# Kernel tuning notes

Hardware: AMD Instinct MI355X
Metric: run time of the kernel (lower is better)

The kernel has to match this reference:

```python
import jax, jax.numpy as jnp
import numpy as np

D_MODEL, D_K, D_V, HEADS = 512, 8, 8, 6
EPS = 1e-5


def setup_inputs() -> dict:
    key = jax.random.key(0)
    ks = jax.random.split(key, 16)
    B, S = 16, 1024
    inp = {
        'q_input': jax.random.normal(ks[0], (B, S, D_MODEL), jnp.float32),
        'k_input': jax.random.normal(ks[1], (B, S, D_MODEL), jnp.float32),
        'v_input': jax.random.normal(ks[2], (B, S, D_MODEL), jnp.float32),
        'mask': jax.random.randint(ks[3], (B, S, S), 0, 2).astype(bool),
        'Wq': jax.random.normal(ks[4], (D_MODEL, D_K * HEADS), jnp.float32) * 0.04,
        'bq': jax.random.normal(ks[5], (D_K * HEADS,), jnp.float32) * 0.02,
        'Wk': jax.random.normal(ks[6], (D_MODEL, D_K * HEADS), jnp.float32) * 0.04,
        'bk': jax.random.normal(ks[7], (D_K * HEADS,), jnp.float32) * 0.02,
        'Wv': jax.random.normal(ks[8], (D_MODEL, D_V * HEADS), jnp.float32) * 0.04,
        'bv': jax.random.normal(ks[9], (D_V * HEADS,), jnp.float32) * 0.02,
        'Wo': jax.random.normal(ks[10], (HEADS * D_K, D_MODEL), jnp.float32) * 0.1,
        'bo': jax.random.normal(ks[11], (D_MODEL,), jnp.float32) * 0.02,
        'ln_w': 1.0 + jax.random.normal(ks[12], (D_MODEL,), jnp.float32) * 0.02,
        'ln_b': jax.random.normal(ks[13], (D_MODEL,), jnp.float32) * 0.02,
    }
    return inp


def reference(q_input, k_input, v_input, mask, Wq, bq, Wk, bk, Wv, bv, Wo, bo, ln_w, ln_b):
    B, S, _ = q_input.shape
    # projections -> [B, H, S, d]
    q_s = (q_input @ Wq + bq).reshape(B, S, HEADS, D_K).transpose(0, 2, 1, 3)
    k_s = (k_input @ Wk + bk).reshape(B, S, HEADS, D_K).transpose(0, 2, 1, 3)
    v_s = (v_input @ Wv + bv).reshape(B, S, HEADS, D_V).transpose(0, 2, 1, 3)
    # scaled dot-product with masked_fill(mask, 1e-9) as in the original (fills VALUE, not -inf)
    scores = jnp.einsum('bhqd,bhkd->bhqk', q_s, k_s) / np.sqrt(D_K).astype(np.float32)
    scores = jnp.where(mask[:, None, :, :], jnp.float32(1e-9), scores)
    attn = jax.nn.softmax(scores, axis=-1)
    out = jnp.einsum('bhqk,bhkd->bhqd', attn, v_s)  # [B,H,S,d_v]
    out = out.transpose(0, 2, 1, 3).reshape(B, S, HEADS * D_K)
    out = out @ Wo + bo
    x = q_input + out  # residual
    mu = jnp.mean(x, axis=-1, keepdims=True)
    var = jnp.var(x, axis=-1, keepdims=True)
    return (x - mu) * jax.lax.rsqrt(var + EPS) * ln_w + ln_b
```

## Files before the change

kernel.cpp:

```cpp
#include <hip/hip_runtime.h>

constexpr int B = 16;
constexpr int S = 1024;
constexpr int DM = 512;
constexpr int H = 6;
constexpr int DK = 8;
constexpr int NJ = H * DK;
constexpr int BS = B * S;
constexpr int WB_ELEMS = 16 * NJ * 32;

typedef __attribute__((ext_vector_type(8))) short bf16x8;
typedef __attribute__((ext_vector_type(8))) _Float16 half8;
typedef __attribute__((ext_vector_type(4))) _Float16 half4;
typedef __attribute__((ext_vector_type(4))) float floatx4;

#define LOG2E 1.4426950408889634f
#define QSCALE (0.35355339059327373f * LOG2E)

__device__ inline ushort f2bf(float f) {
  unsigned int u = __builtin_bit_cast(unsigned int, f);
  return (ushort)((u + 0x7FFFu + ((u >> 16) & 1u)) >> 16);
}

__global__ __launch_bounds__(256) void maskbits_kernel(
    const int* __restrict__ mask, unsigned long long* __restrict__ bits) {
  int wave = threadIdx.x >> 6, lane = threadIdx.x & 63;
  int row = blockIdx.x * 4 + wave;
  const int* mrow = mask + (size_t)row * S;
  unsigned long long* brow = bits + (size_t)row * 16;
  int koff = ((lane >> 5) << 5) + 2 * (lane & 15) + ((lane >> 4) & 1);
#pragma unroll
  for (int c = 0; c < 16; c++) {
    int v = mrow[c * 64 + koff];
    unsigned long long bal = __ballot(v != 0);
    if (lane == 0) brow[c] = bal;
  }
}

__global__ __launch_bounds__(256) void wprep_kernel(
    const float* __restrict__ Wq, const float* __restrict__ Wk,
    const float* __restrict__ Wv, ushort* __restrict__ Wb,
    uint2* __restrict__ VBf) {
  int m = blockIdx.x;
  if (m < 3) {
    const float* W = (m == 0) ? Wq : (m == 1) ? Wk : Wv;
    ushort* dst = Wb + (size_t)m * WB_ELEMS;
    for (int e = threadIdx.x; e < WB_ELEMS; e += 256) {
      int kc = e / 1536;
      int rem = e - kc * 1536;
      int n = rem >> 5, kj = rem & 31;
      dst[e] = f2bf(W[(size_t)(kc * 32 + kj) * NJ + n]);
    }
  } else {
    int bh = m - 3;
    for (int i = threadIdx.x; i < 2048; i += 256) {
      int tile = i >> 5;
      int li = i & 31;
      int g = li >> 3, dd = 8 + (li & 7);
      uint hv = (dd == 8) ? 0x3C003C00u : 0u;
      uint2 val; val.x = hv; val.y = hv;
      VBf[((size_t)bh * 64 + tile) * 64 + g * 16 + dd] = val;
    }
  }
}

__global__ __launch_bounds__(256) void proj_kernel(
    const float* __restrict__ q_in, const float* __restrict__ k_in,
    const float* __restrict__ v_in, const ushort* __restrict__ Wb,
    const float* __restrict__ bq, const float* __restrict__ bk,
    const float* __restrict__ bv,
    ushort* __restrict__ Qo, ushort* __restrict__ Ko, ushort* __restrict__ Vo) {
  int m = blockIdx.y;
  const float* x    = (m == 0) ? q_in : (m == 1) ? k_in : v_in;
  const float* bias = (m == 0) ? bq   : (m == 1) ? bk   : bv;
  ushort* out       = (m == 0) ? Qo   : (m == 1) ? Ko   : Vo;
  float oscale      = (m == 0) ? QSCALE : 1.0f;
  const ushort* Wg  = Wb + (size_t)m * WB_ELEMS;

  __shared__ ushort Wl[WB_ELEMS];

  int t = threadIdx.x;
  {
    const uint4* src = (const uint4*)Wg;
    uint4* dst = (uint4*)Wl;
#pragma unroll
    for (int i = 0; i < 12; i++) dst[t + i * 256] = src[t + i * 256];
  }

  int r0 = blockIdx.x * 64;
  int wave = t >> 6, lane = t & 63;
  int n16 = lane & 15, quad = lane >> 4;
  const float* xrow = x + (size_t)(r0 + wave * 16 + n16) * DM + quad * 8;

  floatx4 acc0 = {0.f, 0.f, 0.f, 0.f};
  floatx4 acc1 = {0.f, 0.f, 0.f, 0.f};
  floatx4 acc2 = {0.f, 0.f, 0.f, 0.f};

  __syncthreads();

#pragma unroll 4
  for (int kc = 0; kc < 16; kc++) {
    float4 xa = *(const float4*)(xrow + kc * 32);
    float4 xb = *(const float4*)(xrow + kc * 32 + 4);
    bf16x8 a;
    a[0] = (short)f2bf(xa.x); a[1] = (short)f2bf(xa.y);
    a[2] = (short)f2bf(xa.z); a[3] = (short)f2bf(xa.w);
    a[4] = (short)f2bf(xb.x); a[5] = (short)f2bf(xb.y);
    a[6] = (short)f2bf(xb.z); a[7] = (short)f2bf(xb.w);
    const ushort* wbase = &Wl[(kc * 48 + n16) * 32 + quad * 8];
    bf16x8 b0 = *(const bf16x8*)(wbase);
    bf16x8 b1 = *(const bf16x8*)(wbase + 16 * 32);
    bf16x8 b2 = *(const bf16x8*)(wbase + 32 * 32);
    acc0 = __builtin_amdgcn_mfma_f32_16x16x32_bf16(a, b0, acc0, 0, 0, 0);
    acc1 = __builtin_amdgcn_mfma_f32_16x16x32_bf16(a, b1, acc1, 0, 0, 0);
    acc2 = __builtin_amdgcn_mfma_f32_16x16x32_bf16(a, b2, acc2, 0, 0, 0);
  }

  int baseR = r0 + wave * 16 + quad * 4;
#pragma unroll
  for (int j = 0; j < 3; j++) {
    floatx4 a = (j == 0) ? acc0 : (j == 1) ? acc1 : acc2;
    int n = j * 16 + n16;
    float bn = bias[n];
    int h = n >> 3, d = n & 7;
#pragma unroll
    for (int r = 0; r < 4; r++) {
      int R = baseR + r;
      int b = R >> 10, s = R & 1023;
      float fv = (a[r] + bn) * oscale;
      if (m == 2) {
        size_t idx =
            ((((size_t)(b * H + h) * 64 + (s >> 4)) * 64) +
             ((s >> 2) & 3) * 16 + d) * 4 + (s & 3);
        out[idx] = __builtin_bit_cast(ushort, (_Float16)fv);
      } else {
        out[(((size_t)(b * H + h)) * S + s) * 8 + d] = f2bf(fv);
      }
    }
  }
}

__global__ __launch_bounds__(256, 6) void attn_kernel(
    const ushort* __restrict__ Qg, const ushort* __restrict__ Kg,
    const ushort* __restrict__ VBg ,
    const uint* __restrict__ bits32, float* __restrict__ A) {
  int bh = blockIdx.x >> 4;
  int qt = blockIdx.x & 15;
  int b = bh / H, h = bh % H;
  int q0 = qt * 64;

  int t = threadIdx.x;
  int wave = t >> 6, lane = t & 63;
  int quad = lane >> 4, n16 = lane & 15;

  const ushort* Kbase = Kg + (size_t)bh * S * 8;
  const uint2* VB = (const uint2*)VBg + (size_t)bh * (64 * 64);

  bf16x8 aq = {0, 0, 0, 0, 0, 0, 0, 0};
  if (quad == 0)
    aq = *(const bf16x8*)&Qg[((size_t)bh * S + q0 + wave * 16 + n16) * 8];

  const uint* mrow = bits32 + (size_t)(b * S + q0 + wave * 16 + n16) * 32;

  floatx4 acc0 = {0.f, 0.f, 0.f, 0.f};
  floatx4 acc1 = {0.f, 0.f, 0.f, 0.f};
  const floatx4 zero = {0.f, 0.f, 0.f, 0.f};
  int sh0 = 2 * quad;

#pragma unroll 1
  for (int cc = 0; cc < 8; cc++) {
    uint4 mq = *(const uint4*)(mrow + cc * 4);
#pragma unroll
    for (int ci = 0; ci < 4; ci++) {
      int c = cc * 4 + ci;
      uint mw = (ci == 0) ? mq.x : (ci == 1) ? mq.y : (ci == 2) ? mq.z : mq.w;

      bf16x8 ak0 = *(const bf16x8*)&Kbase[(size_t)(c * 32 + n16) * 8];
      bf16x8 ak1 = *(const bf16x8*)&Kbase[(size_t)(c * 32 + 16 + n16) * 8];
      uint2 vb0 = VB[(2 * c) * 64 + lane];
      uint2 vb1 = VB[(2 * c + 1) * 64 + lane];

      floatx4 s0 = __builtin_amdgcn_mfma_f32_16x16x32_bf16(ak0, aq, zero, 0, 0, 0);
      floatx4 s1 = __builtin_amdgcn_mfma_f32_16x16x32_bf16(ak1, aq, zero, 0, 0, 0);

      float p0 = exp2f(fminf(s0[0], 15.f)), p1 = exp2f(fminf(s0[1], 15.f));
      float p2 = exp2f(fminf(s0[2], 15.f)), p3 = exp2f(fminf(s0[3], 15.f));
      float p4 = exp2f(fminf(s1[0], 15.f)), p5 = exp2f(fminf(s1[1], 15.f));
      float p6 = exp2f(fminf(s1[2], 15.f)), p7 = exp2f(fminf(s1[3], 15.f));
      uint w0 = __builtin_bit_cast(uint, __builtin_amdgcn_cvt_pkrtz(p0, p1));
      uint w1 = __builtin_bit_cast(uint, __builtin_amdgcn_cvt_pkrtz(p2, p3));
      uint w2 = __builtin_bit_cast(uint, __builtin_amdgcn_cvt_pkrtz(p4, p5));
      uint w3 = __builtin_bit_cast(uint, __builtin_amdgcn_cvt_pkrtz(p6, p7));

      uint m0 = ((mw >> sh0) & 0x10001u) * 0xFFFFu;
      uint m1 = ((mw >> (sh0 + 1)) & 0x10001u) * 0xFFFFu;
      uint m2 = ((mw >> (sh0 + 8)) & 0x10001u) * 0xFFFFu;
      uint m3 = ((mw >> (sh0 + 9)) & 0x10001u) * 0xFFFFu;
      w0 = (m0 & 0x3C003C00u) | (~m0 & w0);
      w1 = (m1 & 0x3C003C00u) | (~m1 & w1);
      w2 = (m2 & 0x3C003C00u) | (~m2 & w2);
      w3 = (m3 & 0x3C003C00u) | (~m3 & w3);

      uint2 pu0; pu0.x = w0; pu0.y = w1;
      uint2 pu1; pu1.x = w2; pu1.y = w3;
      half4 pa0 = __builtin_bit_cast(half4, pu0);
      half4 pa1 = __builtin_bit_cast(half4, pu1);

      acc0 = __builtin_amdgcn_mfma_f32_16x16x16f16(
          pa0, __builtin_bit_cast(half4, vb0), acc0, 0, 0, 0);
      acc1 = __builtin_amdgcn_mfma_f32_16x16x16f16(
          pa1, __builtin_bit_cast(half4, vb1), acc1, 0, 0, 0);
    }
  }

#pragma unroll
  for (int r = 0; r < 4; r++) {
    float sum = acc0[r] + acc1[r];
    float dnm = __shfl(sum, (lane & 48) | 8, 64);
    if (n16 < 8) {
      int qg = q0 + wave * 16 + quad * 4 + r;
      A[((size_t)(b * S + qg)) * NJ + h * 8 + n16] = sum / dnm;
    }
  }
}

__global__ __launch_bounds__(256) void out_ln_kernel(
    const float* __restrict__ A, const float* __restrict__ Wo,
    const float* __restrict__ bo, const float* __restrict__ qin,
    const float* __restrict__ lnw, const float* __restrict__ lnb,
    float* __restrict__ out) {
  int r0 = blockIdx.x * 8;
  int t = threadIdx.x;
  __shared__ float As[8 * NJ];
#pragma unroll
  for (int i = t; i < 8 * NJ; i += 256) As[i] = A[(size_t)r0 * NJ + i];
  __syncthreads();

  int c0 = t, c1 = t + 256;
  float acc0[8], acc1[8];
#pragma unroll
  for (int r = 0; r < 8; r++) { acc0[r] = 0.f; acc1[r] = 0.f; }

#pragma unroll 4
  for (int j = 0; j < NJ; j++) {
    float w0 = Wo[(size_t)j * DM + c0];
    float w1 = Wo[(size_t)j * DM + c1];
#pragma unroll
    for (int r = 0; r < 8; r++) {
      float a = As[r * NJ + j];
      acc0[r] += a * w0;
      acc1[r] += a * w1;
    }
  }

  float b0 = bo[c0], b1 = bo[c1];
  float y0[8], y1[8], ssum[8], sq[8];
#pragma unroll
  for (int r = 0; r < 8; r++) {
    y0[r] = acc0[r] + b0 + qin[(size_t)(r0 + r) * DM + c0];
    y1[r] = acc1[r] + b1 + qin[(size_t)(r0 + r) * DM + c1];
    ssum[r] = y0[r] + y1[r];
    sq[r] = y0[r] * y0[r] + y1[r] * y1[r];
  }

  int wave = t >> 6, lane = t & 63;
  __shared__ float reds[4][8], redq[4][8];
#pragma unroll
  for (int r = 0; r < 8; r++) {
    float s = ssum[r], qq = sq[r];
#pragma unroll
    for (int off = 32; off > 0; off >>= 1) {
      s += __shfl_xor(s, off, 64);
      qq += __shfl_xor(qq, off, 64);
    }
    if (lane == 0) { reds[wave][r] = s; redq[wave][r] = qq; }
  }
  __syncthreads();

  float lw0 = lnw[c0], lw1 = lnw[c1], lb0 = lnb[c0], lb1 = lnb[c1];
#pragma unroll
  for (int r = 0; r < 8; r++) {
    float s = (reds[0][r] + reds[1][r]) + (reds[2][r] + reds[3][r]);
    float qq = (redq[0][r] + redq[1][r]) + (redq[2][r] + redq[3][r]);
    float mu = s * (1.f / 512.f);
    float var = qq * (1.f / 512.f) - mu * mu;
    float rstd = rsqrtf(var + 1e-5f);
    out[(size_t)(r0 + r) * DM + c0] = (y0[r] - mu) * rstd * lw0 + lb0;
    out[(size_t)(r0 + r) * DM + c1] = (y1[r] - mu) * rstd * lw1 + lb1;
  }
}

extern "C" void kernel_launch(void* const* d_in, const int* in_sizes, int n_in,
                              void* d_out, int out_size, void* d_ws,
                              size_t ws_size, hipStream_t stream) {
  const float* q_in = (const float*)d_in[0];
  const float* k_in = (const float*)d_in[1];
  const float* v_in = (const float*)d_in[2];
  const int* mask = (const int*)d_in[3];
  const float* Wq = (const float*)d_in[4];
  const float* bq = (const float*)d_in[5];
  const float* Wk = (const float*)d_in[6];
  const float* bk = (const float*)d_in[7];
  const float* Wv = (const float*)d_in[8];
  const float* bv = (const float*)d_in[9];
  const float* Wo = (const float*)d_in[10];
  const float* bo = (const float*)d_in[11];
  const float* lnw = (const float*)d_in[12];
  const float* lnb = (const float*)d_in[13];
  float* out = (float*)d_out;

  constexpr size_t QKV = (size_t)B * H * S * DK;
  ushort* base = (ushort*)d_ws;
  ushort* Qw = base;
  ushort* Kw = base + QKV;
  ushort* VBw = base + 2 * QKV;
  float* Aw = (float*)(base + 4 * QKV);
  unsigned long long* bits = (unsigned long long*)(Aw + (size_t)BS * NJ);
  ushort* Wb = (ushort*)(bits + (size_t)BS * 16);

  maskbits_kernel<<<BS / 4, 256, 0, stream>>>(mask, bits);
  wprep_kernel<<<3 + B * H, 256, 0, stream>>>(Wq, Wk, Wv, Wb, (uint2*)VBw);
  proj_kernel<<<dim3(BS / 64, 3), 256, 0, stream>>>(
      q_in, k_in, v_in, Wb, bq, bk, bv, Qw, Kw, VBw);
  attn_kernel<<<(B * H * S) / 64, 256, 0, stream>>>(
      Qw, Kw, VBw, (const uint*)bits, Aw);
  out_ln_kernel<<<BS / 8, 256, 0, stream>>>(Aw, Wo, bo, q_in, lnw, lnb, out);
}
```

Before: 305.9 us.

## Stage K/V tiles in LDS for attention and prefetch activations in projection

The attention kernel now copies the whole per-head K (16 KB) and V (32 KB) block into shared memory once per workgroup and reads from LDS in the inner loop, replacing repeated global/L2 reads. The inner loop is also fully unrolled. Occupancy hint drops from 6 to 3 blocks per CU to fit the 48 KB of LDS. The projection kernel software-prefetches activation rows four steps ahead, issuing the first loads before the weight copy to overlap latency. The trade-offs are lower occupancy and a serial load phase before compute in attention.

New measurement: 307.5 us. Within noise of the previous version (+0.5%).

```diff
diff --git a/kernel.cpp b/kernel.cpp
--- a/kernel.cpp
+++ b/kernel.cpp
@@ -80,28 +80,39 @@
   __shared__ ushort Wl[WB_ELEMS];
 
   int t = threadIdx.x;
-  {
-    const uint4* src = (const uint4*)Wg;
-    uint4* dst = (uint4*)Wl;
-#pragma unroll
-    for (int i = 0; i < 12; i++) dst[t + i * 256] = src[t + i * 256];
-  }
-
   int r0 = blockIdx.x * 64;
   int wave = t >> 6, lane = t & 63;
   int n16 = lane & 15, quad = lane >> 4;
   const float* xrow = x + (size_t)(r0 + wave * 16 + n16) * DM + quad * 8;
 
+  float4 pa[4], pb[4];
+#pragma unroll
+  for (int i = 0; i < 4; i++) {
+    pa[i] = *(const float4*)(xrow + i * 32);
+    pb[i] = *(const float4*)(xrow + i * 32 + 4);
+  }
+
+  {
+    const uint4* src = (const uint4*)Wg;
+    uint4* dst = (uint4*)Wl;
+#pragma unroll
+    for (int i = 0; i < 12; i++) dst[t + i * 256] = src[t + i * 256];
+  }
+
   floatx4 acc0 = {0.f, 0.f, 0.f, 0.f};
   floatx4 acc1 = {0.f, 0.f, 0.f, 0.f};
   floatx4 acc2 = {0.f, 0.f, 0.f, 0.f};
 
   __syncthreads();
 
-#pragma unroll 4
+#pragma unroll
   for (int kc = 0; kc < 16; kc++) {
-    float4 xa = *(const float4*)(xrow + kc * 32);
-    float4 xb = *(const float4*)(xrow + kc * 32 + 4);
+    float4 xa = pa[kc & 3];
+    float4 xb = pb[kc & 3];
+    if (kc + 4 < 16) {
+      pa[kc & 3] = *(const float4*)(xrow + (kc + 4) * 32);
+      pb[kc & 3] = *(const float4*)(xrow + (kc + 4) * 32 + 4);
+    }
     bf16x8 a;
     a[0] = (short)f2bf(xa.x); a[1] = (short)f2bf(xa.y);
     a[2] = (short)f2bf(xa.z); a[3] = (short)f2bf(xa.w);
@@ -140,7 +151,7 @@
   }
 }
 
-__global__ __launch_bounds__(256, 6) void attn_kernel(
+__global__ __launch_bounds__(256, 3) void attn_kernel(
     const ushort* __restrict__ Qg, const ushort* __restrict__ Kg,
     const ushort* __restrict__ VBg ,
     const uint* __restrict__ bits32, float* __restrict__ A) {
@@ -149,25 +160,39 @@
   int b = bh / H, h = bh % H;
   int q0 = qt * 64;
 
+  __shared__ uint4 Kl[1024];
+  __shared__ uint2 Vl[64 * 64];
+
   int t = threadIdx.x;
   int wave = t >> 6, lane = t & 63;
   int quad = lane >> 4, n16 = lane & 15;
 
-  const ushort* Kbase = Kg + (size_t)bh * S * 8;
-  const uint2* VB = (const uint2*)VBg + (size_t)bh * (64 * 64);
+  {
+    const uint4* Ksrc = (const uint4*)(Kg + (size_t)bh * S * 8);
+#pragma unroll
+    for (int i = 0; i < 4; i++) Kl[t + i * 256] = Ksrc[t + i * 256];
+    const uint2* Vsrc = (const uint2*)VBg + (size_t)bh * (64 * 64);
+#pragma unroll
+    for (int i = 0; i < 16; i++) Vl[t + i * 256] = Vsrc[t + i * 256];
+  }
 
   bf16x8 aq = {0, 0, 0, 0, 0, 0, 0, 0};
   if (quad == 0)
     aq = *(const bf16x8*)&Qg[((size_t)bh * S + q0 + wave * 16 + n16) * 8];
 
   const uint* mrow = bits32 + (size_t)(b * S + q0 + wave * 16 + n16) * 32;
+
+  __syncthreads();
 
   floatx4 acc0 = {0.f, 0.f, 0.f, 0.f};
   floatx4 acc1 = {0.f, 0.f, 0.f, 0.f};
   const floatx4 zero = {0.f, 0.f, 0.f, 0.f};
   int sh0 = 2 * quad;
 
-#pragma unroll 1
+  const ushort* kb = (const ushort*)Kl + n16 * 8;
+  const uint2* vbb = Vl + lane;
+
+#pragma unroll
   for (int cc = 0; cc < 8; cc++) {
     uint4 mq = *(const uint4*)(mrow + cc * 4);
 #pragma unroll
@@ -175,10 +200,10 @@
       int c = cc * 4 + ci;
       uint mw = (ci == 0) ? mq.x : (ci == 1) ? mq.y : (ci == 2) ? mq.z : mq.w;
 
-      bf16x8 ak0 = *(const bf16x8*)&Kbase[(size_t)(c * 32 + n16) * 8];
-      bf16x8 ak1 = *(const bf16x8*)&Kbase[(size_t)(c * 32 + 16 + n16) * 8];
-      uint2 vb0 = VB[(2 * c) * 64 + lane];
-      uint2 vb1 = VB[(2 * c + 1) * 64 + lane];
+      bf16x8 ak0 = *(const bf16x8*)(kb + c * 256);
+      bf16x8 ak1 = *(const bf16x8*)(kb + c * 256 + 128);
+      uint2 vb0 = vbb[(2 * c) * 64];
+      uint2 vb1 = vbb[(2 * c + 1) * 64];
 
       floatx4 s0 = __builtin_amdgcn_mfma_f32_16x16x32_bf16(ak0, aq, zero, 0, 0, 0);
       floatx4 s1 = __builtin_amdgcn_mfma_f32_16x16x32_bf16(ak1, aq, zero, 0, 0, 0);
```
